# Kernel optimization log

Hardware: AMD Instinct MI355X
Metric: run time of the kernel (lower is better)

The kernel has to match this reference:

```python
import jax, jax.numpy as jnp
import numpy as np

NUM_HEADS = 16
CHUNK = 128  # module's chunk_size; softmax is computed PER key-chunk (not globally) as in the source


def setup_inputs() -> dict:
    key = jax.random.key(0)
    ks = jax.random.split(key, 6)
    B, N, C = 2, 2048, 1024
    s = 0.02
    return {
        "x": jax.random.normal(ks[0], (B, N, C), dtype=jnp.float32),
        "Wq": jax.random.normal(ks[1], (C, C), dtype=jnp.float32) * s,
        "Wk": jax.random.normal(ks[2], (C, C), dtype=jnp.float32) * s,
        "Wv": jax.random.normal(ks[3], (C, C), dtype=jnp.float32) * s,
        "Wp": jax.random.normal(ks[4], (C, C), dtype=jnp.float32) * s,
        "bp": jnp.zeros((C,), dtype=jnp.float32),
    }


def reference(x, Wq, Wk, Wv, Wp, bp):
    B, N, C = x.shape
    H = NUM_HEADS
    D = C // H
    scale = jnp.asarray(D, x.dtype) ** -0.5
    # projections (no qkv bias)
    q = (x @ Wq).reshape(B, N, H, D).transpose(0, 2, 1, 3)  # [B,H,N,D]
    k = (x @ Wk).reshape(B, N, H, D).transpose(0, 2, 1, 3)
    v = (x @ Wv).reshape(B, N, H, D).transpose(0, 2, 1, 3)
    # split keys/values into chunks of CHUNK along sequence
    nk = N // CHUNK
    kc = k.reshape(B, H, nk, CHUNK, D)
    vc = v.reshape(B, H, nk, CHUNK, D)
    # scores per key chunk: [B,H,N,nk,CHUNK]
    scores = jnp.einsum('bhnd,bhkcd->bhnkc', q, kc) * scale
    # NOTE: faithful to the source, softmax normalizes within EACH key chunk only
    attn = jax.nn.softmax(scores, axis=-1)
    # accumulate over all key chunks (the += in the torch loop)
    out = jnp.einsum('bhnkc,bhkcd->bhnd', attn, vc)  # [B,H,N,D]
    out = out.transpose(0, 2, 1, 3).reshape(B, N, C)
    return out @ Wp + bp
```

## Files before the change

### kernel.cpp

```cpp
#include <hip/hip_runtime.h>
#include <hip/hip_bf16.h>


typedef __attribute__((ext_vector_type(4))) float f32x4;
typedef __attribute__((ext_vector_type(8))) short short8;

static __device__ __forceinline__ unsigned short f2bfu(float f) {
    union { __hip_bfloat16 b; unsigned short u; } cv;
    cv.b = __float2bfloat16(f);
    return cv.u;
}
static __device__ __forceinline__ __hip_bfloat16 f2bf(float f) {
    return __float2bfloat16(f);
}
static __device__ __forceinline__ unsigned int pkrnd(float a, float b) {
    union { float f; unsigned int u; } ua, ub;
    ua.f = a; ub.f = b;
    return __builtin_amdgcn_perm(ub.u + 0x8000u, ua.u + 0x8000u, 0x07060302u);
}
static __device__ __forceinline__ void gload_lds16(const __hip_bfloat16* g, __hip_bfloat16* l) {
    __builtin_amdgcn_global_load_lds(
        (const __attribute__((address_space(1))) void*)g,
        (__attribute__((address_space(3))) void*)l, 16, 0, 0);
}

__global__ __launch_bounds__(256) void conv_fused_kernel(
    const float* __restrict__ x, __hip_bfloat16* __restrict__ xb,
    const float* __restrict__ w0, const float* __restrict__ w1,
    const float* __restrict__ w2, const float* __restrict__ w3,
    __hip_bfloat16* __restrict__ wt) {
    const int t = threadIdx.x;
    if (blockIdx.x < 4096) {
        int i = blockIdx.x * 256 + t;
        float4 v = ((const float4*)x)[i];
        ushort4 o;
        o.x = f2bfu(v.x); o.y = f2bfu(v.y); o.z = f2bfu(v.z); o.w = f2bfu(v.w);
        ((ushort4*)xb)[i] = o;
    } else {
        __shared__ float tile[32][33];
        int zz = blockIdx.x - 4096;
        int z = zz >> 10, byi = (zz >> 5) & 31, bxi = zz & 31;
        const float* W = (z == 0) ? w0 : (z == 1) ? w1 : (z == 2) ? w2 : w3;
        __hip_bfloat16* out = wt + (size_t)z * 1048576;
        const int tx = t & 31, ty = t >> 5;
        const int r0 = byi * 32, c0 = bxi * 32;
        for (int j = 0; j < 4; ++j)
            tile[ty + j * 8][tx] = W[(size_t)(r0 + ty + j * 8) * 1024 + c0 + tx];
        __syncthreads();
        for (int j = 0; j < 4; ++j)
            out[(size_t)(c0 + ty + j * 8) * 1024 + r0 + tx] = f2bf(tile[tx][ty + j * 8]);
    }
}

__global__ __launch_bounds__(256) void gemm_qkv_kernel(
    const __hip_bfloat16* __restrict__ A, const __hip_bfloat16* __restrict__ WT,
    __hip_bfloat16* __restrict__ q_ws, __hip_bfloat16* __restrict__ k_ws,
    __hip_bfloat16* __restrict__ vT_ws) {
    const int t = threadIdx.x;
    const int lane = t & 63, w = t >> 6;
    const int quad = lane >> 4, l16 = lane & 15;
    const int wm = w >> 1, wn = w & 1;
    const int n0 = blockIdx.x * 128, m0 = blockIdx.y * 128;
    const int z = blockIdx.z;
    const __hip_bfloat16* Bt = WT + (size_t)z * 1048576;

    __shared__ __align__(16) __hip_bfloat16 As[128 * 32];
    __shared__ __align__(16) __hip_bfloat16 Bs[128 * 32];

    const int rS = t >> 2;
    const int cS = ((t & 3) ^ ((t >> 3) & 3)) * 8;
    const __hip_bfloat16* gA = A + (size_t)(m0 + rS) * 1024 + cS;
    const __hip_bfloat16* gB = Bt + (size_t)(n0 + rS) * 1024 + cS;
    __hip_bfloat16* lA = As + (t & 192) * 8;
    __hip_bfloat16* lB = Bs + (t & 192) * 8;
    const int csw = (quad ^ ((l16 >> 1) & 3)) * 8;

    f32x4 acc[4][4];
    const f32x4 z4 = {0.f, 0.f, 0.f, 0.f};
    for (int i = 0; i < 4; ++i)
        for (int j = 0; j < 4; ++j) acc[i][j] = z4;

    for (int kk = 0; kk < 32; ++kk) {
        const int k0 = kk * 32;
        __syncthreads();
        gload_lds16(gA + k0, lA);
        gload_lds16(gA + 64 * 1024 + k0, lA + 256 * 8);
        gload_lds16(gB + k0, lB);
        gload_lds16(gB + 64 * 1024 + k0, lB + 256 * 8);
        __syncthreads();
        short8 af[4], bf[4];
        for (int i = 0; i < 4; ++i)
            af[i] = *(const short8*)(As + (wm * 64 + i * 16 + l16) * 32 + csw);
        for (int j = 0; j < 4; ++j)
            bf[j] = *(const short8*)(Bs + (wn * 64 + j * 16 + l16) * 32 + csw);
        for (int i = 0; i < 4; ++i)
            for (int j = 0; j < 4; ++j)
                acc[i][j] = __builtin_amdgcn_mfma_f32_16x16x32_bf16(af[i], bf[j], acc[i][j], 0, 0, 0);
    }

    const int r0 = m0 + wm * 64, c0 = n0 + wn * 64;
    if (z < 2) {
        const float sc = (z == 0) ? 0.18033688f : 1.0f;
        __hip_bfloat16* dst = (z == 0) ? q_ws : k_ws;
        for (int i = 0; i < 4; ++i) {
            int rowb = r0 + i * 16 + quad * 4;
            for (int j = 0; j < 4; ++j) {
                int col = c0 + j * 16 + l16;
                for (int rg = 0; rg < 4; ++rg)
                    dst[(size_t)(rowb + rg) * 1024 + col] = f2bf(acc[i][j][rg] * sc);
            }
        }
    } else {
        int b = r0 >> 11;
        for (int i = 0; i < 4; ++i) {
            int n_ = (r0 + i * 16 + quad * 4) & 2047;
            int nb = n_ & ~127;
            int c = n_ & 127;
            int vcol = (c & ~31) | (((c >> 2) & 3) << 3) | (((c >> 4) & 1) << 2);
            for (int j = 0; j < 4; ++j) {
                int col = c0 + j * 16 + l16;
                int h = col >> 6, d = col & 63;
                ushort4 o;
                o.x = f2bfu(acc[i][j][0]); o.y = f2bfu(acc[i][j][1]);
                o.z = f2bfu(acc[i][j][2]); o.w = f2bfu(acc[i][j][3]);
                *(ushort4*)(vT_ws + (size_t)((b * 16 + h) * 64 + d) * 2048 + nb + vcol) = o;
            }
        }
    }
}

__global__ __launch_bounds__(256) void gemm_final_kernel(
    const __hip_bfloat16* __restrict__ A, const __hip_bfloat16* __restrict__ Bt,
    float* __restrict__ outF, const float* __restrict__ bias) {
    const int t = threadIdx.x;
    const int lane = t & 63, w = t >> 6;
    const int quad = lane >> 4, l16 = lane & 15;
    const int n0 = blockIdx.x * 128, m0 = blockIdx.y * 64;

    __shared__ __align__(16) __hip_bfloat16 As[64 * 32];
    __shared__ __align__(16) __hip_bfloat16 Bs[128 * 32];

    const int rS = t >> 2;
    const int cS = ((t & 3) ^ ((t >> 3) & 3)) * 8;
    const __hip_bfloat16* gA = A + (size_t)(m0 + rS) * 1024 + cS;
    const __hip_bfloat16* gB = Bt + (size_t)(n0 + rS) * 1024 + cS;
    __hip_bfloat16* lA = As + (t & 192) * 8;
    __hip_bfloat16* lB = Bs + (t & 192) * 8;
    const int csw = (quad ^ ((l16 >> 1) & 3)) * 8;

    f32x4 acc[4][2];
    const f32x4 z4 = {0.f, 0.f, 0.f, 0.f};
    for (int i = 0; i < 4; ++i)
        for (int j = 0; j < 2; ++j) acc[i][j] = z4;

    for (int kk = 0; kk < 32; ++kk) {
        const int k0 = kk * 32;
        __syncthreads();
        gload_lds16(gA + k0, lA);
        gload_lds16(gB + k0, lB);
        gload_lds16(gB + 64 * 1024 + k0, lB + 256 * 8);
        __syncthreads();
        short8 af[4], bf[2];
        for (int i = 0; i < 4; ++i)
            af[i] = *(const short8*)(As + (i * 16 + l16) * 32 + csw);
        for (int j = 0; j < 2; ++j)
            bf[j] = *(const short8*)(Bs + (w * 32 + j * 16 + l16) * 32 + csw);
        for (int i = 0; i < 4; ++i)
            for (int j = 0; j < 2; ++j)
                acc[i][j] = __builtin_amdgcn_mfma_f32_16x16x32_bf16(af[i], bf[j], acc[i][j], 0, 0, 0);
    }

    for (int i = 0; i < 4; ++i) {
        int rowb = m0 + i * 16 + quad * 4;
        for (int j = 0; j < 2; ++j) {
            int col = n0 + w * 32 + j * 16 + l16;
            float bv = bias[col];
            for (int rg = 0; rg < 4; ++rg)
                outF[(size_t)(rowb + rg) * 1024 + col] = acc[i][j][rg] + bv;
        }
    }
}

__global__ __launch_bounds__(256, 2) void attn_kernel(
    const __hip_bfloat16* __restrict__ q_ws, const __hip_bfloat16* __restrict__ k_ws,
    const __hip_bfloat16* __restrict__ vT_ws, __hip_bfloat16* __restrict__ attn_ws) {
    const int t = threadIdx.x, lane = t & 63, w = t >> 6;
    const int quad = lane >> 4, l16 = lane & 15;
    const int qt = blockIdx.x;
    const int bh = blockIdx.y;
    const int b = bh >> 4, h = bh & 15;
    const int q0 = qt * 128;

    __shared__ __align__(16) char smem[71680];

    short8 qf[2][2];
#pragma unroll
    for (int mt = 0; mt < 2; ++mt)
#pragma unroll
        for (int kt = 0; kt < 2; ++kt)
            qf[mt][kt] = *(const short8*)(q_ws + (size_t)(b * 2048 + q0 + w * 32 + mt * 16 + l16) * 1024 + h * 64 + kt * 32 + quad * 8);

    const f32x4 z4 = {0.f, 0.f, 0.f, 0.f};
    f32x4 O[2][4];
#pragma unroll
    for (int mt = 0; mt < 2; ++mt)
#pragma unroll
        for (int dt = 0; dt < 4; ++dt) O[mt][dt] = z4;

    {
        __hip_bfloat16* Ksb = (__hip_bfloat16*)(smem);
        __hip_bfloat16* Vtb = (__hip_bfloat16*)(smem + 18432);
#pragma unroll
        for (int it = 0; it < 4; ++it) {
            int idx = it * 256 + t;
            int r = idx >> 3, sg = idx & 7;
            uint4 v = *(const uint4*)(k_ws + (size_t)(b * 2048 + r) * 1024 + h * 64 + sg * 8);
            *(uint4*)(Ksb + r * 72 + sg * 8) = v;
        }
#pragma unroll
        for (int it = 0; it < 4; ++it) {
            int idx = it * 256 + t;
            int d = idx >> 4, sg = idx & 15;
            uint4 v = *(const uint4*)(vT_ws + (size_t)(bh * 64 + d) * 2048 + sg * 8);
            *(uint4*)(Vtb + d * 136 + sg * 8) = v;
        }
    }
    __syncthreads();

    for (int ck = 0; ck < 16; ++ck) {
        const int cur = ck & 1;
        __hip_bfloat16* Ks = (__hip_bfloat16*)(smem + cur * 35840);
        __hip_bfloat16* Vt = (__hip_bfloat16*)(smem + cur * 35840 + 18432);

        if (ck + 1 < 16) {
            __hip_bfloat16* Ksn = (__hip_bfloat16*)(smem + (cur ^ 1) * 35840);
            __hip_bfloat16* Vtn = (__hip_bfloat16*)(smem + (cur ^ 1) * 35840 + 18432);
            const int nk0 = (ck + 1) * 128;
#pragma unroll
            for (int it = 0; it < 4; ++it) {
                int idx = it * 256 + t;
                int r = idx >> 3, sg = idx & 7;
                uint4 v = *(const uint4*)(k_ws + (size_t)(b * 2048 + nk0 + r) * 1024 + h * 64 + sg * 8);
                *(uint4*)(Ksn + r * 72 + sg * 8) = v;
            }
#pragma unroll
            for (int it = 0; it < 4; ++it) {
                int idx = it * 256 + t;
                int d = idx >> 4, sg = idx & 15;
                uint4 v = *(const uint4*)(vT_ws + (size_t)(bh * 64 + d) * 2048 + nk0 + sg * 8);
                *(uint4*)(Vtn + d * 136 + sg * 8) = v;
            }
        }

        f32x4 s[2][8];
#pragma unroll
        for (int mt = 0; mt < 2; ++mt)
#pragma unroll
            for (int i = 0; i < 8; ++i) s[mt][i] = z4;
#pragma unroll
        for (int kt = 0; kt < 2; ++kt)
#pragma unroll
            for (int i = 0; i < 8; ++i) {
                short8 kf = *(const short8*)(Ks + (i * 16 + l16) * 72 + kt * 32 + quad * 8);
                s[0][i] = __builtin_amdgcn_mfma_f32_16x16x32_bf16(kf, qf[0][kt], s[0][i], 0, 0, 0);
                s[1][i] = __builtin_amdgcn_mfma_f32_16x16x32_bf16(kf, qf[1][kt], s[1][i], 0, 0, 0);
            }

        float inv[2];
#pragma unroll
        for (int mt = 0; mt < 2; ++mt) {
            float sum = 0.f;
#pragma unroll
            for (int i = 0; i < 8; ++i) {
                f32x4 p;
                p[0] = __builtin_amdgcn_exp2f(s[mt][i][0]);
                p[1] = __builtin_amdgcn_exp2f(s[mt][i][1]);
                p[2] = __builtin_amdgcn_exp2f(s[mt][i][2]);
                p[3] = __builtin_amdgcn_exp2f(s[mt][i][3]);
                s[mt][i] = p;
                sum += (p[0] + p[1]) + (p[2] + p[3]);
            }
            sum += __shfl_xor(sum, 16, 64);
            sum += __shfl_xor(sum, 32, 64);
            inv[mt] = 1.0f / sum;
        }

#pragma unroll
        for (int kt = 0; kt < 4; ++kt) {
            short8 bfr[2];
#pragma unroll
            for (int mt = 0; mt < 2; ++mt) {
                union { uint4 u; short8 s8; } bb;
                bb.u.x = pkrnd(s[mt][2 * kt][0] * inv[mt], s[mt][2 * kt][1] * inv[mt]);
                bb.u.y = pkrnd(s[mt][2 * kt][2] * inv[mt], s[mt][2 * kt][3] * inv[mt]);
                bb.u.z = pkrnd(s[mt][2 * kt + 1][0] * inv[mt], s[mt][2 * kt + 1][1] * inv[mt]);
                bb.u.w = pkrnd(s[mt][2 * kt + 1][2] * inv[mt], s[mt][2 * kt + 1][3] * inv[mt]);
                bfr[mt] = bb.s8;
            }
#pragma unroll
            for (int dt = 0; dt < 4; ++dt) {
                short8 vf = *(const short8*)(Vt + (dt * 16 + l16) * 136 + kt * 32 + quad * 8);
                O[0][dt] = __builtin_amdgcn_mfma_f32_16x16x32_bf16(vf, bfr[0], O[0][dt], 0, 0, 0);
                O[1][dt] = __builtin_amdgcn_mfma_f32_16x16x32_bf16(vf, bfr[1], O[1][dt], 0, 0, 0);
            }
        }
        __syncthreads();
    }

    __hip_bfloat16* T = (__hip_bfloat16*)smem;
#pragma unroll
    for (int mt = 0; mt < 2; ++mt)
#pragma unroll
        for (int dt = 0; dt < 4; ++dt) {
            unsigned int w0 = pkrnd(O[mt][dt][0], O[mt][dt][1]);
            unsigned int w1 = pkrnd(O[mt][dt][2], O[mt][dt][3]);
            int drow = dt * 16 + quad * 4;
            *(unsigned int*)(T + (w * 32 + mt * 16 + l16) * 72 + drow) = w0;
            *(unsigned int*)(T + (w * 32 + mt * 16 + l16) * 72 + drow + 2) = w1;
        }
    __syncthreads();
#pragma unroll
    for (int it = 0; it < 4; ++it) {
        int idx = it * 256 + t;
        int q = idx >> 3, seg = idx & 7;
        uint4 vv = *(const uint4*)(T + q * 72 + seg * 8);
        *(uint4*)(attn_ws + (size_t)(b * 2048 + q0 + q) * 1024 + h * 64 + seg * 8) = vv;
    }
}

extern "C" void kernel_launch(void* const* d_in, const int* in_sizes, int n_in,
                              void* d_out, int out_size, void* d_ws, size_t ws_size,
                              hipStream_t stream) {
    const float* x  = (const float*)d_in[0];
    const float* Wq = (const float*)d_in[1];
    const float* Wk = (const float*)d_in[2];
    const float* Wv = (const float*)d_in[3];
    const float* Wp = (const float*)d_in[4];
    const float* bp = (const float*)d_in[5];
    float* out = (float*)d_out;

    char* ws = (char*)d_ws;
    __hip_bfloat16* xb    = (__hip_bfloat16*)(ws);
    __hip_bfloat16* wT    = (__hip_bfloat16*)(ws + 8388608);
    __hip_bfloat16* q_ws  = (__hip_bfloat16*)(ws + 16777216);
    __hip_bfloat16* k_ws  = (__hip_bfloat16*)(ws + 25165824);
    __hip_bfloat16* vT_ws = (__hip_bfloat16*)(ws + 33554432);
    __hip_bfloat16* at_ws = (__hip_bfloat16*)(ws + 41943040);

    conv_fused_kernel<<<8192, 256, 0, stream>>>(x, xb, Wq, Wk, Wv, Wp, wT);
    gemm_qkv_kernel<<<dim3(8, 32, 3), 256, 0, stream>>>(xb, wT, q_ws, k_ws, vT_ws);
    attn_kernel<<<dim3(16, 32), 256, 0, stream>>>(q_ws, k_ws, vT_ws, at_ws);
    gemm_final_kernel<<<dim3(8, 64), 256, 0, stream>>>(at_ws, wT + 3 * 1048576, out, bp);
}
```

Before: 184.6 us.

## Split attention warps across query and key halves with XOR-swizzled LDS tiles

Reorganises the attention kernel so each warp handles 64 queries against half of each 128-key chunk, instead of 32 queries against the whole chunk. Per-chunk softmax sums are combined across the two key-half warps through a small shared buffer, and the partial outputs are reduced through LDS at the end. K and V tiles now use XOR-swizzled unpadded LDS layouts, and the next chunk is prefetched into registers and written to LDS after the mid-iteration barrier. The aim is more reuse of each K/V fragment across query tiles and fewer bank conflicts. The cost is an extra barrier per chunk, more registers for four query tiles, and a final cross-warp reduction.

```diff
diff --git a/kernel.cpp b/kernel.cpp
--- a/kernel.cpp
+++ b/kernel.cpp
@@ -186,145 +186,187 @@
     const __hip_bfloat16* __restrict__ vT_ws, __hip_bfloat16* __restrict__ attn_ws) {
     const int t = threadIdx.x, lane = t & 63, w = t >> 6;
     const int quad = lane >> 4, l16 = lane & 15;
+    const int qg = w & 1, kg = w >> 1;
     const int qt = blockIdx.x;
     const int bh = blockIdx.y;
     const int b = bh >> 4, h = bh & 15;
     const int q0 = qt * 128;
 
-    __shared__ __align__(16) char smem[71680];
-
-    short8 qf[2][2];
-#pragma unroll
-    for (int mt = 0; mt < 2; ++mt)
+    __shared__ __align__(16) char smem[66048];
+    float* ps = (float*)(smem + 65536);
+
+    const int sgK = t & 7, rKl = t >> 3;
+    const int pK = sgK ^ (rKl & 7);
+    const int sgV = t & 15, rVl = t >> 4;
+    const int pV = sgV ^ (rVl & 15);
+    const __hip_bfloat16* gK = k_ws + (size_t)(b * 2048) * 1024 + h * 64;
+    const __hip_bfloat16* gV = vT_ws + (size_t)(bh * 64) * 2048;
+
+    short8 qf[4][2];
+#pragma unroll
+    for (int j = 0; j < 4; ++j)
 #pragma unroll
         for (int kt = 0; kt < 2; ++kt)
-            qf[mt][kt] = *(const short8*)(q_ws + (size_t)(b * 2048 + q0 + w * 32 + mt * 16 + l16) * 1024 + h * 64 + kt * 32 + quad * 8);
+            qf[j][kt] = *(const short8*)(q_ws + (size_t)(b * 2048 + q0 + qg * 64 + j * 16 + l16) * 1024 + h * 64 + kt * 32 + quad * 8);
 
     const f32x4 z4 = {0.f, 0.f, 0.f, 0.f};
-    f32x4 O[2][4];
-#pragma unroll
-    for (int mt = 0; mt < 2; ++mt)
-#pragma unroll
-        for (int dt = 0; dt < 4; ++dt) O[mt][dt] = z4;
+    f32x4 O[4][4];
+#pragma unroll
+    for (int j = 0; j < 4; ++j)
+#pragma unroll
+        for (int dt = 0; dt < 4; ++dt) O[j][dt] = z4;
 
     {
-        __hip_bfloat16* Ksb = (__hip_bfloat16*)(smem);
-        __hip_bfloat16* Vtb = (__hip_bfloat16*)(smem + 18432);
+        __hip_bfloat16* Ks0 = (__hip_bfloat16*)smem;
+        __hip_bfloat16* Vt0 = (__hip_bfloat16*)(smem + 16384);
+#pragma unroll
+        for (int it = 0; it < 4; ++it) {
+            int r = it * 32 + rKl;
+            uint4 v = *(const uint4*)(gK + (size_t)r * 1024 + sgK * 8);
+            *(uint4*)(Ks0 + r * 64 + pK * 8) = v;
+        }
+#pragma unroll
+        for (int it = 0; it < 4; ++it) {
+            int r = it * 16 + rVl;
+            uint4 v = *(const uint4*)(gV + (size_t)r * 2048 + sgV * 8);
+            *(uint4*)(Vt0 + r * 128 + pV * 8) = v;
+        }
+    }
+    __syncthreads();
+
+    for (int ck = 0; ck < 16; ++ck) {
+        const int cur = ck & 1;
+        __hip_bfloat16* Ks = (__hip_bfloat16*)(smem + cur * 32768);
+        __hip_bfloat16* Vt = (__hip_bfloat16*)(smem + cur * 32768 + 16384);
+
+        uint4 stK[4], stV[4];
+        if (ck < 15) {
+#pragma unroll
+            for (int it = 0; it < 4; ++it)
+                stK[it] = *(const uint4*)(gK + (size_t)((ck + 1) * 128 + it * 32 + rKl) * 1024 + sgK * 8);
+#pragma unroll
+            for (int it = 0; it < 4; ++it)
+                stV[it] = *(const uint4*)(gV + (size_t)(it * 16 + rVl) * 2048 + (ck + 1) * 128 + sgV * 8);
+        }
+
+        f32x4 s[4][4];
+#pragma unroll
+        for (int j = 0; j < 4; ++j)
+#pragma unroll
+            for (int i = 0; i < 4; ++i) s[j][i] = z4;
+#pragma unroll
+        for (int kt = 0; kt < 2; ++kt) {
+            short8 kf[4];
+#pragma unroll
+            for (int i = 0; i < 4; ++i)
+                kf[i] = *(const short8*)(Ks + (kg * 64 + i * 16 + l16) * 64 + (((kt * 4 + quad) ^ (l16 & 7)) * 8));
+#pragma unroll
+            for (int i = 0; i < 4; ++i)
+#pragma unroll
+                for (int j = 0; j < 4; ++j)
+                    s[j][i] = __builtin_amdgcn_mfma_f32_16x16x32_bf16(kf[i], qf[j][kt], s[j][i], 0, 0, 0);
+        }
+
+        float own[4];
+#pragma unroll
+        for (int j = 0; j < 4; ++j) {
+            float sum = 0.f;
+#pragma unroll
+            for (int i = 0; i < 4; ++i) {
+                f32x4 p;
+                p[0] = __builtin_amdgcn_exp2f(s[j][i][0]);
+                p[1] = __builtin_amdgcn_exp2f(s[j][i][1]);
+                p[2] = __builtin_amdgcn_exp2f(s[j][i][2]);
+                p[3] = __builtin_amdgcn_exp2f(s[j][i][3]);
+                s[j][i] = p;
+                sum += (p[0] + p[1]) + (p[2] + p[3]);
+            }
+            sum += __shfl_xor(sum, 16, 64);
+            sum += __shfl_xor(sum, 32, 64);
+            own[j] = sum;
+        }
+        if (quad == 0) {
+#pragma unroll
+            for (int j = 0; j < 4; ++j)
+                ps[(kg * 8 + qg * 4 + j) * 16 + l16] = own[j];
+        }
+        __syncthreads();
+
+        if (ck < 15) {
+            __hip_bfloat16* Ksn = (__hip_bfloat16*)(smem + (cur ^ 1) * 32768);
+            __hip_bfloat16* Vtn = (__hip_bfloat16*)(smem + (cur ^ 1) * 32768 + 16384);
+#pragma unroll
+            for (int it = 0; it < 4; ++it)
+                *(uint4*)(Ksn + (it * 32 + rKl) * 64 + pK * 8) = stK[it];
+#pragma unroll
+            for (int it = 0; it < 4; ++it)
+                *(uint4*)(Vtn + (it * 16 + rVl) * 128 + pV * 8) = stV[it];
+        }
+
+        float inv[4];
+#pragma unroll
+        for (int j = 0; j < 4; ++j)
+            inv[j] = 1.0f / (own[j] + ps[((kg ^ 1) * 8 + qg * 4 + j) * 16 + l16]);
+
+#pragma unroll
+        for (int ktl = 0; ktl < 2; ++ktl) {
+            short8 bfr[4];
+#pragma unroll
+            for (int j = 0; j < 4; ++j) {
+                const int i0 = 2 * ktl, i1 = 2 * ktl + 1;
+                union { uint4 u; short8 s8; } bb;
+                bb.u.x = pkrnd(s[j][i0][0] * inv[j], s[j][i0][1] * inv[j]);
+                bb.u.y = pkrnd(s[j][i0][2] * inv[j], s[j][i0][3] * inv[j]);
+                bb.u.z = pkrnd(s[j][i1][0] * inv[j], s[j][i1][1] * inv[j]);
+                bb.u.w = pkrnd(s[j][i1][2] * inv[j], s[j][i1][3] * inv[j]);
+                bfr[j] = bb.s8;
+            }
+#pragma unroll
+            for (int dt = 0; dt < 4; ++dt) {
+                short8 vf = *(const short8*)(Vt + (dt * 16 + l16) * 128 + ((((kg * 2 + ktl) * 4 + quad) ^ l16) * 8));
+#pragma unroll
+                for (int j = 0; j < 4; ++j)
+                    O[j][dt] = __builtin_amdgcn_mfma_f32_16x16x32_bf16(vf, bfr[j], O[j][dt], 0, 0, 0);
+            }
+        }
+        __syncthreads();
+    }
+
+    if (kg == 1) {
+        float* Of = (float*)(smem + qg * 16384);
+#pragma unroll
+        for (int dt = 0; dt < 4; ++dt)
+#pragma unroll
+            for (int j = 0; j < 4; ++j)
+                *(f32x4*)(Of + ((size_t)((dt * 4 + j) * 64 + quad * 16 + l16)) * 4) = O[j][dt];
+    }
+    __syncthreads();
+    if (kg == 0) {
+        float* Of = (float*)(smem + qg * 16384);
+        __hip_bfloat16* T = (__hip_bfloat16*)(smem + 32768);
+#pragma unroll
+        for (int dt = 0; dt < 4; ++dt)
+#pragma unroll
+            for (int j = 0; j < 4; ++j) {
+                f32x4 o2 = *(const f32x4*)(Of + ((size_t)((dt * 4 + j) * 64 + quad * 16 + l16)) * 4);
+                f32x4 oo = O[j][dt] + o2;
+                unsigned int w0 = pkrnd(oo[0], oo[1]);
+                unsigned int w1 = pkrnd(oo[2], oo[3]);
+                int r = qg * 64 + j * 16 + l16;
+                *(unsigned int*)(T + r * 72 + dt * 16 + quad * 4) = w0;
+                *(unsigned int*)(T + r * 72 + dt * 16 + quad * 4 + 2) = w1;
+            }
+    }
+    __syncthreads();
+    {
+        const __hip_bfloat16* T = (const __hip_bfloat16*)(smem + 32768);
 #pragma unroll
         for (int it = 0; it < 4; ++it) {
             int idx = it * 256 + t;
-            int r = idx >> 3, sg = idx & 7;
-            uint4 v = *(const uint4*)(k_ws + (size_t)(b * 2048 + r) * 1024 + h * 64 + sg * 8);
-            *(uint4*)(Ksb + r * 72 + sg * 8) = v;
-        }
-#pragma unroll
-        for (int it = 0; it < 4; ++it) {
-            int idx = it * 256 + t;
-            int d = idx >> 4, sg = idx & 15;
-            uint4 v = *(const uint4*)(vT_ws + (size_t)(bh * 64 + d) * 2048 + sg * 8);
-            *(uint4*)(Vtb + d * 136 + sg * 8) = v;
-        }
-    }
-    __syncthreads();
-
-    for (int ck = 0; ck < 16; ++ck) {
-        const int cur = ck & 1;
-        __hip_bfloat16* Ks = (__hip_bfloat16*)(smem + cur * 35840);
-        __hip_bfloat16* Vt = (__hip_bfloat16*)(smem + cur * 35840 + 18432);
-
-        if (ck + 1 < 16) {
-            __hip_bfloat16* Ksn = (__hip_bfloat16*)(smem + (cur ^ 1) * 35840);
-            __hip_bfloat16* Vtn = (__hip_bfloat16*)(smem + (cur ^ 1) * 35840 + 18432);
-            const int nk0 = (ck + 1) * 128;
-#pragma unroll
-            for (int it = 0; it < 4; ++it) {
-                int idx = it * 256 + t;
-                int r = idx >> 3, sg = idx & 7;
-                uint4 v = *(const uint4*)(k_ws + (size_t)(b * 2048 + nk0 + r) * 1024 + h * 64 + sg * 8);
-                *(uint4*)(Ksn + r * 72 + sg * 8) = v;
-            }
-#pragma unroll
-            for (int it = 0; it < 4; ++it) {
-                int idx = it * 256 + t;
-                int d = idx >> 4, sg = idx & 15;
-                uint4 v = *(const uint4*)(vT_ws + (size_t)(bh * 64 + d) * 2048 + nk0 + sg * 8);
-                *(uint4*)(Vtn + d * 136 + sg * 8) = v;
-            }
-        }
-
-        f32x4 s[2][8];
-#pragma unroll
-        for (int mt = 0; mt < 2; ++mt)
-#pragma unroll
-            for (int i = 0; i < 8; ++i) s[mt][i] = z4;
-#pragma unroll
-        for (int kt = 0; kt < 2; ++kt)
-#pragma unroll
-            for (int i = 0; i < 8; ++i) {
-                short8 kf = *(const short8*)(Ks + (i * 16 + l16) * 72 + kt * 32 + quad * 8);
-                s[0][i] = __builtin_amdgcn_mfma_f32_16x16x32_bf16(kf, qf[0][kt], s[0][i], 0, 0, 0);
-                s[1][i] = __builtin_amdgcn_mfma_f32_16x16x32_bf16(kf, qf[1][kt], s[1][i], 0, 0, 0);
-            }
-
-        float inv[2];
-#pragma unroll
-        for (int mt = 0; mt < 2; ++mt) {
-            float sum = 0.f;
-#pragma unroll
-            for (int i = 0; i < 8; ++i) {
-                f32x4 p;
-                p[0] = __builtin_amdgcn_exp2f(s[mt][i][0]);
-                p[1] = __builtin_amdgcn_exp2f(s[mt][i][1]);
-                p[2] = __builtin_amdgcn_exp2f(s[mt][i][2]);
-                p[3] = __builtin_amdgcn_exp2f(s[mt][i][3]);
-                s[mt][i] = p;
-                sum += (p[0] + p[1]) + (p[2] + p[3]);
-            }
-            sum += __shfl_xor(sum, 16, 64);
-            sum += __shfl_xor(sum, 32, 64);
-            inv[mt] = 1.0f / sum;
-        }
-
-#pragma unroll
-        for (int kt = 0; kt < 4; ++kt) {
-            short8 bfr[2];
-#pragma unroll
-            for (int mt = 0; mt < 2; ++mt) {
-                union { uint4 u; short8 s8; } bb;
-                bb.u.x = pkrnd(s[mt][2 * kt][0] * inv[mt], s[mt][2 * kt][1] * inv[mt]);
-                bb.u.y = pkrnd(s[mt][2 * kt][2] * inv[mt], s[mt][2 * kt][3] * inv[mt]);
-                bb.u.z = pkrnd(s[mt][2 * kt + 1][0] * inv[mt], s[mt][2 * kt + 1][1] * inv[mt]);
-                bb.u.w = pkrnd(s[mt][2 * kt + 1][2] * inv[mt], s[mt][2 * kt + 1][3] * inv[mt]);
-                bfr[mt] = bb.s8;
-            }
-#pragma unroll
-            for (int dt = 0; dt < 4; ++dt) {
-                short8 vf = *(const short8*)(Vt + (dt * 16 + l16) * 136 + kt * 32 + quad * 8);
-                O[0][dt] = __builtin_amdgcn_mfma_f32_16x16x32_bf16(vf, bfr[0], O[0][dt], 0, 0, 0);
-                O[1][dt] = __builtin_amdgcn_mfma_f32_16x16x32_bf16(vf, bfr[1], O[1][dt], 0, 0, 0);
-            }
-        }
-        __syncthreads();
-    }
-
-    __hip_bfloat16* T = (__hip_bfloat16*)smem;
-#pragma unroll
-    for (int mt = 0; mt < 2; ++mt)
-#pragma unroll
-        for (int dt = 0; dt < 4; ++dt) {
-            unsigned int w0 = pkrnd(O[mt][dt][0], O[mt][dt][1]);
-            unsigned int w1 = pkrnd(O[mt][dt][2], O[mt][dt][3]);
-            int drow = dt * 16 + quad * 4;
-            *(unsigned int*)(T + (w * 32 + mt * 16 + l16) * 72 + drow) = w0;
-            *(unsigned int*)(T + (w * 32 + mt * 16 + l16) * 72 + drow + 2) = w1;
-        }
-    __syncthreads();
-#pragma unroll
-    for (int it = 0; it < 4; ++it) {
-        int idx = it * 256 + t;
-        int q = idx >> 3, seg = idx & 7;
-        uint4 vv = *(const uint4*)(T + q * 72 + seg * 8);
-        *(uint4*)(attn_ws + (size_t)(b * 2048 + q0 + q) * 1024 + h * 64 + seg * 8) = vv;
+            int q = idx >> 3, seg = idx & 7;
+            uint4 vv = *(const uint4*)(T + q * 72 + seg * 8);
+            *(uint4*)(attn_ws + (size_t)(b * 2048 + q0 + q) * 1024 + h * 64 + seg * 8) = vv;
+        }
     }
 }
 
```

Result: slower. 228.6 us (+23.8%).
